# Optimization experiments

Measured on AMD Instinct MI355X. Metric: run time of the kernel, lower is better.

The kernel has to match this reference:

```python
import jax, jax.numpy as jnp
import numpy as np

CHANNELS = 256
C_QK = CHANNELS // 8


def setup_inputs() -> dict:
    key = jax.random.key(0)
    ks = jax.random.split(key, 7)
    b, c, h, w = 8, CHANNELS, 64, 64
    x = jax.random.normal(ks[0], (b, c, h, w), dtype=jnp.float32)
    # 1x1 conv weights stored as [out_ch, in_ch]; biases [out_ch]
    s = 1.0 / np.sqrt(c)
    wq = jax.random.uniform(ks[1], (C_QK, c), jnp.float32, -s, s)
    bq = jax.random.uniform(ks[2], (C_QK,), jnp.float32, -s, s)
    wk = jax.random.uniform(ks[3], (C_QK, c), jnp.float32, -s, s)
    bk = jax.random.uniform(ks[4], (C_QK,), jnp.float32, -s, s)
    wv = jax.random.uniform(ks[5], (c, c), jnp.float32, -s, s)
    bv = jax.random.uniform(ks[6], (c,), jnp.float32, -s, s)
    return {"x": x, "wq": wq, "bq": bq, "wk": wk, "bk": bk, "wv": wv, "bv": bv}


def reference(x, wq, bq, wk, bk, wv, bv):
    b, c, h, w = x.shape
    xf = x.reshape(b, c, h * w)  # [b, c, n]
    # 1x1 convs == per-pixel linear projections
    q = jnp.einsum('oc,bcn->bon', wq, xf) + bq[None, :, None]  # [b, c//8, n]
    k = jnp.einsum('oc,bcn->bon', wk, xf) + bk[None, :, None]  # [b, c//8, n]
    v = jnp.einsum('oc,bcn->bon', wv, xf) + bv[None, :, None]  # [b, c, n]
    # attention[i, j] = q_i . k_j  (no scaling, matching the torch code)
    attn = jnp.einsum('bdi,bdj->bij', q, k)  # [b, n, n]
    attn = jax.nn.softmax(attn, axis=-1)
    # out[:, :, i] = sum_j attn[i, j] * v[:, :, j]
    out = jnp.einsum('bij,bcj->bci', attn, v)  # [b, c, n]
    return out.reshape(b, c, h, w)
```

## Files before the change

### kernel.cpp

```cpp
#include <hip/hip_runtime.h>
#include <stdint.h>

#define NB 8
#define NC 256
#define ND 32
#define NN 4096
#define QT 64
#define KT 32
#define NBUF 4

typedef __attribute__((ext_vector_type(8))) short short8;
typedef __attribute__((ext_vector_type(4))) float float4_;

#define MFMA16(a,b,c) __builtin_amdgcn_mfma_f32_16x16x32_bf16((a),(b),(c),0,0,0)

#if __has_builtin(__builtin_amdgcn_exp2f)
#define EXP2(x) __builtin_amdgcn_exp2f(x)
#else
#define EXP2(x) exp2f(x)
#endif
#define L2E 1.44269504088896f
#define SCB (24.0f * L2E)

__device__ __forceinline__ uint16_t f2bf(float f) {
  uint32_t u = __builtin_bit_cast(uint32_t, f);
  u += 0x7fffu + ((u >> 16) & 1u);
  return (uint16_t)(u >> 16);
}
__device__ __forceinline__ float bf2f(uint16_t h) {
  uint32_t u = (uint32_t)h << 16;
  return __builtin_bit_cast(float, u);
}
__device__ __forceinline__ short8 ld8(const uint16_t* p) {
  return *reinterpret_cast<const short8*>(p);
}
__device__ __forceinline__ uint32_t cvtpk(float lo, float hi) {
  uint32_t r;
  asm("v_cvt_pk_bf16_f32 %0, %1, %2" : "=v"(r) : "v"(lo), "v"(hi));
  return r;
}
__device__ __forceinline__ void async16(const uint16_t* g, uint16_t* l) {
  __builtin_amdgcn_global_load_lds(
      (const __attribute__((address_space(1))) uint32_t*)g,
      (__attribute__((address_space(3))) uint32_t*)l, 16, 0, 0);
}
__device__ __forceinline__ void fbar() {
  asm volatile("" ::: "memory");
  __builtin_amdgcn_s_barrier();
  asm volatile("" ::: "memory");
}

__global__ __launch_bounds__(256) void k_prep(
    const float* __restrict__ x, const float* __restrict__ wq,
    const float* __restrict__ wk, const float* __restrict__ wv,
    uint16_t* __restrict__ xTh, uint16_t* __restrict__ xTl,
    uint16_t* __restrict__ WhP, uint16_t* __restrict__ WlP, int use_xl)
{
  int bx = blockIdx.x, tid = threadIdx.x;
  if (bx >= 2048) {
    int e = (bx - 2048) * 256 + tid;
    int row = e >> 8, col = e & 255;
    float w = (row < 32) ? wq[e] : (row < 64) ? wk[e - 32 * 256]
                                              : wv[e - 64 * 256];
    uint16_t h = f2bf(w);
    int ks = col >> 5, c5 = col & 31;
    WhP[(size_t)ks * 12800 + row * 40 + c5] = h;
    if (row < 64)
      WlP[(size_t)ks * 2560 + row * 40 + c5] = f2bf(w - bf2f(h));
    return;
  }
  __shared__ uint32_t tile[64][65];
  int b = bx >> 8, t = bx & 255;
  int c0 = (t >> 6) << 6, n0 = (t & 63) << 6;
  const float* xb = x + ((size_t)b * NC + c0) * NN + n0;
  int cc = tid >> 4, nw = (tid & 15) << 2;
  for (int i = 0; i < 4; i++) {
    int c = cc + 16 * i;
    float4_ v = *reinterpret_cast<const float4_*>(xb + (size_t)c * NN + nw);
    for (int u = 0; u < 4; u++) {
      uint16_t h = f2bf(v[u]);
      uint16_t l = f2bf(v[u] - bf2f(h));
      tile[c][nw + u] = (uint32_t)h | ((uint32_t)l << 16);
    }
  }
  __syncthreads();
  int cw = (tid & 15) << 2, nn = tid >> 4;
  for (int i = 0; i < 4; i++) {
    int n = nn + 16 * i;
    uint32_t p0 = tile[cw + 0][n], p1 = tile[cw + 1][n];
    uint32_t p2 = tile[cw + 2][n], p3 = tile[cw + 3][n];
    size_t o = ((size_t)b * NN + n0 + n) * NC + c0 + cw;
    *(uint32_t*)(xTh + o)     = (p0 & 0xffffu) | (p1 << 16);
    *(uint32_t*)(xTh + o + 2) = (p2 & 0xffffu) | (p3 << 16);
    if (use_xl) {
      *(uint32_t*)(xTl + o)     = (p0 >> 16) | (p1 & 0xffff0000u);
      *(uint32_t*)(xTl + o + 2) = (p2 >> 16) | (p3 & 0xffff0000u);
    }
  }
}

__global__ __launch_bounds__(256) void k_qkv(
    const uint16_t* __restrict__ xTh, const uint16_t* __restrict__ xTl,
    const uint16_t* __restrict__ WhP, const uint16_t* __restrict__ WlP,
    const float* __restrict__ bq, const float* __restrict__ bk,
    const float* __restrict__ bv,
    uint16_t* __restrict__ Qh, uint16_t* __restrict__ Ql,
    uint16_t* __restrict__ Kh, uint16_t* __restrict__ Kl,
    uint16_t* __restrict__ V, int use_xl, int use_lo)
{
  __shared__ uint16_t sW[2][15360];

  int b = blockIdx.x & 7, n0 = (blockIdx.x >> 3) * 64;
  int tid = threadIdx.x, wid = tid >> 6, lane = tid & 63;
  int l15 = lane & 15, quad = lane >> 4;
  int nb = n0 + wid * 16;

  auto stageW = [&](int ks, int buf) {
    const uint16_t* srcH = WhP + (size_t)ks * 12800;
    const uint16_t* srcL = WlP + (size_t)ks * 2560;
    uint16_t* dst = &sW[buf][0];
#pragma unroll
    for (int i = 0; i < 8; i++) {
      int idx = i * 256 + tid;
      if (idx < 1920) {
        const uint16_t* g = (idx < 1600) ? (srcH + (size_t)idx * 8)
                                         : (srcL + (size_t)(idx - 1600) * 8);
        async16(g, dst + (size_t)idx * 8);
      }
    }
  };

  float4_ acc[20];
  for (int m = 0; m < 20; m++) acc[m] = (float4_){0.f, 0.f, 0.f, 0.f};

  size_t xa0 = ((size_t)b * NN + nb + l15) * NC + quad * 8;
  short8 bh = ld8(xTh + xa0), blo;
  if (use_xl) blo = ld8(xTl + xa0);

  stageW(0, 0);
  __syncthreads();

  for (int ks = 0; ks < 8; ks++) {
    int buf = ks & 1;
    if (ks < 7) stageW(ks + 1, buf ^ 1);
    short8 nbh, nblo;
    if (ks < 7) {
      size_t xn = xa0 + (size_t)(ks + 1) * 32;
      nbh = ld8(xTh + xn);
      if (use_xl) nblo = ld8(xTl + xn);
    }
    const uint16_t* wb = &sW[buf][0];
#pragma unroll
    for (int mt = 0; mt < 20; mt++) {
      short8 ah = ld8(wb + (16 * mt + l15) * 40 + quad * 8);
      acc[mt] = MFMA16(ah, bh, acc[mt]);
      if (mt < 4) {
        short8 al = ld8(wb + 12800 + (16 * mt + l15) * 40 + quad * 8);
        acc[mt] = MFMA16(al, bh, acc[mt]);
      }
      if (use_xl) acc[mt] = MFMA16(ah, blo, acc[mt]);
    }
    __syncthreads();
    bh = nbh;
    if (use_xl) blo = nblo;
  }

  int n = nb + l15;
  for (int mt = 0; mt < 20; mt++) {
    for (int r = 0; r < 4; r++) {
      int row = 16 * mt + quad * 4 + r;
      float v = acc[mt][r];
      if (mt < 2) {
        v = (v + bq[row]) * L2E;
        size_t o = ((size_t)b * NN + n) * ND + row;
        uint16_t h = f2bf(v);
        Qh[o] = h;
        if (use_lo) Ql[o] = f2bf(v - bf2f(h));
      } else if (mt < 4) {
        int rk = row - 32;
        v += bk[rk];
        size_t o = ((size_t)b * NN + n) * ND + rk;
        uint16_t h = f2bf(v);
        Kh[o] = h;
        if (use_lo) Kl[o] = f2bf(v - bf2f(h));
      } else {
        int c = row - 64;
        v += bv[c];
        V[((size_t)b * NC + c) * NN + n] = f2bf(v);
      }
    }
  }
}

__global__ __launch_bounds__(512, 4) void k_attn(
    const uint16_t* __restrict__ Qh, const uint16_t* __restrict__ Ql,
    const uint16_t* __restrict__ Kh, const uint16_t* __restrict__ Kl,
    const uint16_t* __restrict__ V, float* __restrict__ out, int use_lo)
{
  __shared__ uint16_t sV[NBUF][256][KT];
  __shared__ uint16_t sP[2][4][16][40];
  __shared__ float sL[QT];

  int bx = blockIdx.x;
  int b = bx & 7;
  int q0 = (bx >> 3) * QT;
  int tid = threadIdx.x, wid = tid >> 6, lane = tid & 63;
  int l15 = lane & 15, quad = lane >> 4;
  const size_t qkb = (size_t)b * NN * ND;
  const uint16_t* Vb = V + (size_t)b * NC * NN;
  const bool heavy = (wid < 4);

  int sw = (l15 >> 1) & 3;

  const uint16_t* gp0; const uint16_t* gp1;
  const uint16_t* gp2; const uint16_t* gp3;
  uint32_t off0, off1, off2, off3;
  if (!heavy) {
#define INITGP(i, GP, OFF)                                   \
    { int sl = (wid - 4) * 256 + 64 * i + lane;              \
      int c = sl >> 2;                                       \
      int q2s = (sl & 3) ^ ((sl >> 3) & 3);                  \
      GP = Vb + (size_t)c * NN + q2s * 8;                    \
      OFF = (uint32_t)(((wid - 4) * 4 + i) * 512); }
    INITGP(0, gp0, off0) INITGP(1, gp1, off1)
    INITGP(2, gp2, off2) INITGP(3, gp3, off3)
#undef INITGP
  }
  auto stage = [&](int s) {
    uint16_t* base = &sV[0][0][0] + (size_t)(s & 3) * 8192;
    async16(gp0, base + off0); gp0 += KT;
    async16(gp1, base + off1); gp1 += KT;
    async16(gp2, base + off2); gp2 += KT;
    async16(gp3, base + off3); gp3 += KT;
  };

  float4_ acc[2][4];
  for (int m = 0; m < 2; m++) for (int n = 0; n < 4; n++)
    acc[m][n] = (float4_){0.f, 0.f, 0.f, 0.f};
  float l_part = 0.f;

  short8 qfh, qfl, kh0, kh1, kl0, kl1;
  const uint16_t* pKh = Kh + qkb + (size_t)l15 * ND + quad * 8;
  const uint16_t* pKl = Kl + qkb + (size_t)l15 * ND + quad * 8;

  auto qkt = [&](int sb, short8 h0, short8 h1, short8 lo0, short8 lo1) {
    float4_ S0 = (float4_){0.f, 0.f, 0.f, 0.f}, S1 = S0;
    S0 = MFMA16(h0, qfh, S0);
    S1 = MFMA16(h1, qfh, S1);
    if (use_lo) {
      S0 = MFMA16(lo0, qfh, S0); S0 = MFMA16(h0, qfl, S0);
      S1 = MFMA16(lo1, qfh, S1); S1 = MFMA16(h1, qfl, S1);
    }
    float p0[4], p1[4];
#pragma unroll
    for (int r = 0; r < 4; r++) {
      p0[r] = EXP2(S0[r] - SCB);
      p1[r] = EXP2(S1[r] - SCB);
    }
    l_part += ((p0[0] + p0[1]) + (p0[2] + p0[3])) +
              ((p1[0] + p1[1]) + (p1[2] + p1[3]));
    uint2 w0, w1;
    w0.x = cvtpk(p0[0], p0[1]); w0.y = cvtpk(p0[2], p0[3]);
    w1.x = cvtpk(p1[0], p1[1]); w1.y = cvtpk(p1[2], p1[3]);
    *reinterpret_cast<uint2*>(&sP[sb][wid][l15][4 * quad]) = w0;
    *reinterpret_cast<uint2*>(&sP[sb][wid][l15][16 + 4 * quad]) = w1;
  };

  if (heavy) {
    size_t a = qkb + (size_t)(q0 + wid * 16 + l15) * ND + quad * 8;
    qfh = ld8(Qh + a);
    if (use_lo) qfl = ld8(Ql + a);
    short8 t0 = ld8(pKh), t1 = ld8(pKh + 512), tl0, tl1;
    if (use_lo) { tl0 = ld8(pKl); tl1 = ld8(pKl + 512); }
    qkt(0, t0, t1, tl0, tl1);
    kh0 = ld8(pKh + 1024); kh1 = ld8(pKh + 1536);
    if (use_lo) { kl0 = ld8(pKl + 1024); kl1 = ld8(pKl + 1536); }
    pKh += 2048; pKl += 2048;
    asm volatile("s_waitcnt lgkmcnt(0)" ::: "memory");
  } else {
    stage(0); stage(1); stage(2);
    asm volatile("s_waitcnt vmcnt(8)" ::: "memory");
  }
  fbar();

  for (int j = 0; j < NN / KT; j++) {
    int buf = j & 3;
    int pb = j & 1;
    if (heavy) {
      short8 nh0, nh1, nl0, nl1;
      if (j < NN / KT - 2) {
        nh0 = ld8(pKh); nh1 = ld8(pKh + 512);
        if (use_lo) { nl0 = ld8(pKl); nl1 = ld8(pKl + 512); }
        pKh += 1024; pKl += 1024;
      }
      if (j < NN / KT - 1)
        qkt(pb ^ 1, kh0, kh1, kl0, kl1);
      kh0 = nh0; kh1 = nh1;
      if (use_lo) { kl0 = nl0; kl1 = nl1; }
    } else {
      if (j < NN / KT - 3) stage(j + 3);
    }
    short8 bfP[4];
#pragma unroll
    for (int qt = 0; qt < 4; qt++)
      bfP[qt] = ld8(&sP[pb][qt][l15][quad * 8]);
#pragma unroll
    for (int mt = 0; mt < 2; mt++) {
      short8 af = ld8(&sV[buf][wid * 32 + 16 * mt + l15][(quad ^ sw) * 8]);
#pragma unroll
      for (int qt = 0; qt < 4; qt++)
        acc[mt][qt] = MFMA16(af, bfP[qt], acc[mt][qt]);
    }
    if (!heavy) {
      if (j < NN / KT - 3)
        asm volatile("s_waitcnt vmcnt(8)" ::: "memory");
      else
        asm volatile("s_waitcnt vmcnt(0)" ::: "memory");
    }
    asm volatile("s_waitcnt lgkmcnt(0)" ::: "memory");
    fbar();
  }

  if (heavy) {
    float l_tot = l_part;
    l_tot += __shfl_xor(l_tot, 16);
    l_tot += __shfl_xor(l_tot, 32);
    if (quad == 0) sL[wid * 16 + l15] = l_tot;
  }
  __syncthreads();
  float linv[4];
  for (int qt = 0; qt < 4; qt++) linv[qt] = 1.0f / sL[qt * 16 + l15];
  for (int mt = 0; mt < 2; mt++)
    for (int qt = 0; qt < 4; qt++)
      for (int r = 0; r < 4; r++) {
        int c = wid * 32 + 16 * mt + quad * 4 + r;
        int q = q0 + qt * 16 + l15;
        out[((size_t)(b * NC + c)) * NN + q] = acc[mt][qt][r] * linv[qt];
      }
}

extern "C" void kernel_launch(void* const* d_in, const int* in_sizes, int n_in,
                              void* d_out, int out_size, void* d_ws, size_t ws_size,
                              hipStream_t stream)
{
  const float* x  = (const float*)d_in[0];
  const float* wq = (const float*)d_in[1];
  const float* bq = (const float*)d_in[2];
  const float* wk = (const float*)d_in[3];
  const float* bk = (const float*)d_in[4];
  const float* wv = (const float*)d_in[5];
  const float* bv = (const float*)d_in[6];
  float* out = (float*)d_out;

  const size_t szXT = (size_t)NB * NN * NC * 2;
  const size_t szWh = (size_t)8 * 320 * 40 * 2;
  const size_t szWl = (size_t)8 * 64 * 40 * 2;
  const size_t szQK = (size_t)NB * NN * ND * 2;
  const size_t szV  = (size_t)NB * NC * NN * 2;
  size_t needA = 2 * szXT + szWh + szWl + 4 * szQK + szV;
  size_t needB = szXT + szWh + szWl + 4 * szQK + szV;
  int use_xl = ws_size >= needA;
  int use_lo = ws_size >= needB;

  char* p = (char*)d_ws;
  uint16_t* xTh = (uint16_t*)p; p += szXT;
  uint16_t* xTl = use_xl ? (uint16_t*)p : xTh; if (use_xl) p += szXT;
  uint16_t* WhP = (uint16_t*)p; p += szWh;
  uint16_t* WlP = (uint16_t*)p; p += szWl;
  uint16_t* Qh = (uint16_t*)p; p += szQK;
  uint16_t* Ql = use_lo ? (uint16_t*)p : xTh; if (use_lo) p += szQK;
  uint16_t* Kh = (uint16_t*)p; p += szQK;
  uint16_t* Kl = use_lo ? (uint16_t*)p : xTh; if (use_lo) p += szQK;
  uint16_t* Vw = (uint16_t*)p;

  hipLaunchKernelGGL(k_prep, dim3(2368), dim3(256), 0, stream,
                     x, wq, wk, wv, xTh, xTl, WhP, WlP, use_xl);
  hipLaunchKernelGGL(k_qkv, dim3(512), dim3(256), 0, stream,
                     xTh, xTl, WhP, WlP, bq, bk, bv, Qh, Ql, Kh, Kl, Vw,
                     use_xl, use_lo);
  hipLaunchKernelGGL(k_attn, dim3(512), dim3(512), 0, stream,
                     Qh, Ql, Kh, Kl, Vw, out, use_lo);
}
```

Measured before the change: 246.6 us.

## Fuse x transpose and bf16 split into QKV projection kernel

Moves the fp32-to-bf16 hi/lo split and transpose of x out of the prep kernel and into the QKV kernel, which now transposes 128-channel chunks into shared memory. This removes the global xTh/xTl intermediates and their write-then-read round trip. The weight staging drops from double-buffered to single-buffered with an extra barrier per k-step, which removes load/compute overlap, and the larger shared-memory footprint may reduce occupancy.

New measurement: 235.7 us. 1.05x faster.

```diff
diff --git a/kernel.cpp b/kernel.cpp
--- a/kernel.cpp
+++ b/kernel.cpp
@@ -11,6 +11,7 @@
 
 typedef __attribute__((ext_vector_type(8))) short short8;
 typedef __attribute__((ext_vector_type(4))) float float4_;
+typedef __attribute__((ext_vector_type(4))) unsigned int uint4_;
 
 #define MFMA16(a,b,c) __builtin_amdgcn_mfma_f32_16x16x32_bf16((a),(b),(c),0,0,0)
 
@@ -51,81 +52,63 @@
 }
 
 __global__ __launch_bounds__(256) void k_prep(
-    const float* __restrict__ x, const float* __restrict__ wq,
-    const float* __restrict__ wk, const float* __restrict__ wv,
-    uint16_t* __restrict__ xTh, uint16_t* __restrict__ xTl,
-    uint16_t* __restrict__ WhP, uint16_t* __restrict__ WlP, int use_xl)
+    const float* __restrict__ wq, const float* __restrict__ wk,
+    const float* __restrict__ wv,
+    uint16_t* __restrict__ WhP, uint16_t* __restrict__ WlP)
 {
-  int bx = blockIdx.x, tid = threadIdx.x;
-  if (bx >= 2048) {
-    int e = (bx - 2048) * 256 + tid;
-    int row = e >> 8, col = e & 255;
-    float w = (row < 32) ? wq[e] : (row < 64) ? wk[e - 32 * 256]
-                                              : wv[e - 64 * 256];
-    uint16_t h = f2bf(w);
-    int ks = col >> 5, c5 = col & 31;
-    WhP[(size_t)ks * 12800 + row * 40 + c5] = h;
-    if (row < 64)
-      WlP[(size_t)ks * 2560 + row * 40 + c5] = f2bf(w - bf2f(h));
-    return;
-  }
-  __shared__ uint32_t tile[64][65];
-  int b = bx >> 8, t = bx & 255;
-  int c0 = (t >> 6) << 6, n0 = (t & 63) << 6;
-  const float* xb = x + ((size_t)b * NC + c0) * NN + n0;
-  int cc = tid >> 4, nw = (tid & 15) << 2;
-  for (int i = 0; i < 4; i++) {
-    int c = cc + 16 * i;
-    float4_ v = *reinterpret_cast<const float4_*>(xb + (size_t)c * NN + nw);
-    for (int u = 0; u < 4; u++) {
-      uint16_t h = f2bf(v[u]);
-      uint16_t l = f2bf(v[u] - bf2f(h));
-      tile[c][nw + u] = (uint32_t)h | ((uint32_t)l << 16);
-    }
-  }
-  __syncthreads();
-  int cw = (tid & 15) << 2, nn = tid >> 4;
-  for (int i = 0; i < 4; i++) {
-    int n = nn + 16 * i;
-    uint32_t p0 = tile[cw + 0][n], p1 = tile[cw + 1][n];
-    uint32_t p2 = tile[cw + 2][n], p3 = tile[cw + 3][n];
-    size_t o = ((size_t)b * NN + n0 + n) * NC + c0 + cw;
-    *(uint32_t*)(xTh + o)     = (p0 & 0xffffu) | (p1 << 16);
-    *(uint32_t*)(xTh + o + 2) = (p2 & 0xffffu) | (p3 << 16);
-    if (use_xl) {
-      *(uint32_t*)(xTl + o)     = (p0 >> 16) | (p1 & 0xffff0000u);
-      *(uint32_t*)(xTl + o + 2) = (p2 >> 16) | (p3 & 0xffff0000u);
-    }
-  }
+  int e = blockIdx.x * 256 + threadIdx.x;
+  int row = e >> 8, col = e & 255;
+  float w = (row < 32) ? wq[e] : (row < 64) ? wk[e - 32 * 256]
+                                            : wv[e - 64 * 256];
+  uint16_t h = f2bf(w);
+  int ks = col >> 5, c5 = col & 31;
+  WhP[(size_t)ks * 12800 + row * 40 + c5] = h;
+  if (row < 64)
+    WlP[(size_t)ks * 2560 + row * 40 + c5] = f2bf(w - bf2f(h));
 }
 
 __global__ __launch_bounds__(256) void k_qkv(
-    const uint16_t* __restrict__ xTh, const uint16_t* __restrict__ xTl,
+    const float* __restrict__ x,
     const uint16_t* __restrict__ WhP, const uint16_t* __restrict__ WlP,
     const float* __restrict__ bq, const float* __restrict__ bk,
     const float* __restrict__ bv,
     uint16_t* __restrict__ Qh, uint16_t* __restrict__ Ql,
     uint16_t* __restrict__ Kh, uint16_t* __restrict__ Kl,
-    uint16_t* __restrict__ V, int use_xl, int use_lo)
+    uint16_t* __restrict__ V, int use_lo)
 {
-  __shared__ uint16_t sW[2][15360];
+  __shared__ uint32_t xt[64][132];
+  __shared__ uint16_t sW[15360];
 
   int b = blockIdx.x & 7, n0 = (blockIdx.x >> 3) * 64;
   int tid = threadIdx.x, wid = tid >> 6, lane = tid & 63;
   int l15 = lane & 15, quad = lane >> 4;
-  int nb = n0 + wid * 16;
-
-  auto stageW = [&](int ks, int buf) {
+  int nb = wid * 16;
+
+  auto stageW = [&](int ks) {
     const uint16_t* srcH = WhP + (size_t)ks * 12800;
     const uint16_t* srcL = WlP + (size_t)ks * 2560;
-    uint16_t* dst = &sW[buf][0];
 #pragma unroll
     for (int i = 0; i < 8; i++) {
       int idx = i * 256 + tid;
       if (idx < 1920) {
         const uint16_t* g = (idx < 1600) ? (srcH + (size_t)idx * 8)
                                          : (srcL + (size_t)(idx - 1600) * 8);
-        async16(g, dst + (size_t)idx * 8);
+        async16(g, sW + (size_t)idx * 8);
+      }
+    }
+  };
+  auto transpose = [&](int ch) {
+    const float* xb = x + ((size_t)b * NC + ch * 128) * NN + n0;
+    int cc = tid >> 4, nw = (tid & 15) << 2;
+#pragma unroll
+    for (int i = 0; i < 8; i++) {
+      int c = cc + 16 * i;
+      float4_ v = *reinterpret_cast<const float4_*>(xb + (size_t)c * NN + nw);
+#pragma unroll
+      for (int u = 0; u < 4; u++) {
+        uint16_t h = f2bf(v[u]);
+        uint16_t l = f2bf(v[u] - bf2f(h));
+        xt[nw + u][c] = (uint32_t)h | ((uint32_t)l << 16);
       }
     }
   };
@@ -133,39 +116,45 @@
   float4_ acc[20];
   for (int m = 0; m < 20; m++) acc[m] = (float4_){0.f, 0.f, 0.f, 0.f};
 
-  size_t xa0 = ((size_t)b * NN + nb + l15) * NC + quad * 8;
-  short8 bh = ld8(xTh + xa0), blo;
-  if (use_xl) blo = ld8(xTl + xa0);
-
-  stageW(0, 0);
+  stageW(0);
+  transpose(0);
   __syncthreads();
 
-  for (int ks = 0; ks < 8; ks++) {
-    int buf = ks & 1;
-    if (ks < 7) stageW(ks + 1, buf ^ 1);
-    short8 nbh, nblo;
-    if (ks < 7) {
-      size_t xn = xa0 + (size_t)(ks + 1) * 32;
-      nbh = ld8(xTh + xn);
-      if (use_xl) nblo = ld8(xTl + xn);
-    }
-    const uint16_t* wb = &sW[buf][0];
+  for (int gks = 0; gks < 8; gks++) {
+    int ksl = gks & 3;
+    const uint32_t* xr = &xt[nb + l15][ksl * 32 + quad * 8];
+    uint4_ r0 = *reinterpret_cast<const uint4_*>(xr);
+    uint4_ r1 = *reinterpret_cast<const uint4_*>(xr + 4);
+    uint4_ H, L;
+    H.x = (r0.x & 0xffffu) | (r0.y << 16);
+    L.x = (r0.x >> 16)     | (r0.y & 0xffff0000u);
+    H.y = (r0.z & 0xffffu) | (r0.w << 16);
+    L.y = (r0.z >> 16)     | (r0.w & 0xffff0000u);
+    H.z = (r1.x & 0xffffu) | (r1.y << 16);
+    L.z = (r1.x >> 16)     | (r1.y & 0xffff0000u);
+    H.w = (r1.z & 0xffffu) | (r1.w << 16);
+    L.w = (r1.z >> 16)     | (r1.w & 0xffff0000u);
+    short8 bh  = __builtin_bit_cast(short8, H);
+    short8 blo = __builtin_bit_cast(short8, L);
 #pragma unroll
     for (int mt = 0; mt < 20; mt++) {
-      short8 ah = ld8(wb + (16 * mt + l15) * 40 + quad * 8);
+      short8 ah = ld8(sW + (16 * mt + l15) * 40 + quad * 8);
       acc[mt] = MFMA16(ah, bh, acc[mt]);
       if (mt < 4) {
-        short8 al = ld8(wb + 12800 + (16 * mt + l15) * 40 + quad * 8);
+        short8 al = ld8(sW + 12800 + (16 * mt + l15) * 40 + quad * 8);
         acc[mt] = MFMA16(al, bh, acc[mt]);
       }
-      if (use_xl) acc[mt] = MFMA16(ah, blo, acc[mt]);
+      acc[mt] = MFMA16(ah, blo, acc[mt]);
     }
     __syncthreads();
-    bh = nbh;
-    if (use_xl) blo = nblo;
-  }
-
-  int n = nb + l15;
+    if (gks < 7) {
+      stageW(gks + 1);
+      if (gks == 3) transpose(1);
+      __syncthreads();
+    }
+  }
+
+  int n = n0 + wid * 16 + l15;
   for (int mt = 0; mt < 20; mt++) {
     for (int r = 0; r < 4; r++) {
       int row = 16 * mt + quad * 4 + r;
@@ -352,32 +341,26 @@
   const float* bv = (const float*)d_in[6];
   float* out = (float*)d_out;
 
-  const size_t szXT = (size_t)NB * NN * NC * 2;
   const size_t szWh = (size_t)8 * 320 * 40 * 2;
   const size_t szWl = (size_t)8 * 64 * 40 * 2;
   const size_t szQK = (size_t)NB * NN * ND * 2;
   const size_t szV  = (size_t)NB * NC * NN * 2;
-  size_t needA = 2 * szXT + szWh + szWl + 4 * szQK + szV;
-  size_t needB = szXT + szWh + szWl + 4 * szQK + szV;
-  int use_xl = ws_size >= needA;
+  size_t needB = szWh + szWl + 4 * szQK + szV;
   int use_lo = ws_size >= needB;
 
   char* p = (char*)d_ws;
-  uint16_t* xTh = (uint16_t*)p; p += szXT;
-  uint16_t* xTl = use_xl ? (uint16_t*)p : xTh; if (use_xl) p += szXT;
   uint16_t* WhP = (uint16_t*)p; p += szWh;
   uint16_t* WlP = (uint16_t*)p; p += szWl;
   uint16_t* Qh = (uint16_t*)p; p += szQK;
-  uint16_t* Ql = use_lo ? (uint16_t*)p : xTh; if (use_lo) p += szQK;
+  uint16_t* Ql = use_lo ? (uint16_t*)p : Qh; if (use_lo) p += szQK;
   uint16_t* Kh = (uint16_t*)p; p += szQK;
-  uint16_t* Kl = use_lo ? (uint16_t*)p : xTh; if (use_lo) p += szQK;
+  uint16_t* Kl = use_lo ? (uint16_t*)p : Kh; if (use_lo) p += szQK;
   uint16_t* Vw = (uint16_t*)p;
 
-  hipLaunchKernelGGL(k_prep, dim3(2368), dim3(256), 0, stream,
-                     x, wq, wk, wv, xTh, xTl, WhP, WlP, use_xl);
+  hipLaunchKernelGGL(k_prep, dim3(320), dim3(256), 0, stream,
+                     wq, wk, wv, WhP, WlP);
   hipLaunchKernelGGL(k_qkv, dim3(512), dim3(256), 0, stream,
-                     xTh, xTl, WhP, WlP, bq, bk, bv, Qh, Ql, Kh, Kl, Vw,
-                     use_xl, use_lo);
+                     x, WhP, WlP, bq, bk, bv, Qh, Ql, Kh, Kl, Vw, use_lo);
   hipLaunchKernelGGL(k_attn, dim3(512), dim3(512), 0, stream,
                      Qh, Ql, Kh, Kl, Vw, out, use_lo);
 }
```
